# Kernel tuning notes

Hardware: AMD Instinct MI355X
Metric: run time of the kernel (lower is better)

The kernel has to match this reference:

```python
import jax, jax.numpy as jnp
import numpy as np

L = 65536   # sequence length (keys/values)
D = 512     # embed dim (hardcoded in source)
H = 4       # heads
HD = 128    # head dim

def _ln(x, g, b):
    m = jnp.mean(x, -1, keepdims=True)
    v = jnp.var(x, -1, keepdims=True)
    return (x - m) * jax.lax.rsqrt(v + 1e-5) * g + b

def setup_inputs() -> dict:
    key = jax.random.key(0)
    ks = jax.random.split(key, 6)
    s = 0.02
    return {
        "x": jax.random.normal(ks[0], (L, D), jnp.float32),
        "w_in": jax.random.normal(ks[1], (3 * D, D), jnp.float32) * s,
        "b_in": jnp.zeros((3 * D,), jnp.float32),
        "w_out": jax.random.normal(ks[2], (D, D), jnp.float32) * s,
        "b_out": jnp.zeros((D,), jnp.float32),
        "w1": jax.random.normal(ks[3], (D, D), jnp.float32) * s,
        "b1": jnp.zeros((D,), jnp.float32),
        "w2": jax.random.normal(ks[4], (D, D), jnp.float32) * s,
        "b2": jnp.zeros((D,), jnp.float32),
        "g1": jnp.ones((D,), jnp.float32),
        "be1": jnp.zeros((D,), jnp.float32),
        "g2": jnp.ones((D,), jnp.float32),
        "be2": jnp.zeros((D,), jnp.float32),
    }

def reference(x, w_in, b_in, w_out, b_out, w1, b1, w2, b2, g1, be1, g2, be2):
    xn = _ln(x, g1, be1)                               # [L, D]
    q = xn[:1] @ w_in[:D].T + b_in[:D]                 # [1, D] single-row query
    k = xn @ w_in[D:2 * D].T + b_in[D:2 * D]           # [L, D]
    v = xn @ w_in[2 * D:].T + b_in[2 * D:]             # [L, D]
    qh = q.reshape(H, HD)                              # [H, HD]
    kh = k.reshape(L, H, HD)
    vh = v.reshape(L, H, HD)
    scores = jnp.einsum('hd,lhd->hl', qh, kh) * (1.0 / np.sqrt(HD))  # [H, L]
    attn = jax.nn.softmax(scores, axis=-1)
    o = jnp.einsum('hl,lhd->hd', attn, vh).reshape(1, D)             # [1, D]
    o = o @ w_out.T + b_out
    y = x[:1] + o                                      # residual keeps only row 0
    yn = _ln(y, g2, be2)
    h = jax.nn.relu(yn @ w1.T + b1)
    return y + h @ w2.T + b2                           # [1, D]
```

## Files before the change

### kernel.cpp

```cpp
#include <hip/hip_runtime.h>
#include <math.h>

#define LL 65536
#define DD 512
#define NH 4
#define HDIM 128


__device__ __forceinline__ float dot4(float4 a, float4 b) {
    return a.x * b.x + a.y * b.y + a.z * b.z + a.w * b.w;
}
__device__ __forceinline__ float wred(float v) {
#pragma unroll
    for (int m = 32; m; m >>= 1) v += __shfl_xor(v, m, 64);
    return v;
}
__device__ __forceinline__ float4 f4fma(float4 acc, float s, float4 v) {
    acc.x += s * v.x; acc.y += s * v.y; acc.z += s * v.z; acc.w += s * v.w;
    return acc;
}
__device__ __forceinline__ float4 f4sfma(float4 acc, float c, float s, float4 v) {
    acc.x = acc.x * c + s * v.x; acc.y = acc.y * c + s * v.y;
    acc.z = acc.z * c + s * v.z; acc.w = acc.w * c + s * v.w;
    return acc;
}
__device__ __forceinline__ float4 f4scale(float4 a, float s) {
    a.x *= s; a.y *= s; a.z *= s; a.w *= s; return a;
}
__device__ __forceinline__ float4 lnrm4(float4 v, float m, float r, float4 g, float4 b) {
    float4 o;
    o.x = (v.x - m) * r * g.x + b.x; o.y = (v.y - m) * r * g.y + b.y;
    o.z = (v.z - m) * r * g.z + b.z; o.w = (v.w - m) * r * g.w + b.w;
    return o;
}

__global__ __launch_bounds__(256) void kA1(const float* __restrict__ x,
                                           const float* __restrict__ w_in,
                                           const float* __restrict__ b_in,
                                           const float* __restrict__ g1,
                                           const float* __restrict__ be1,
                                           float* __restrict__ ws) {
    int lane = threadIdx.x & 63;
    int j = blockIdx.x * 4 + (threadIdx.x >> 6);
    const float4* x4 = (const float4*)x;
    float4 a = x4[lane], b = x4[64 + lane];
    float ps = a.x + a.y + a.z + a.w + b.x + b.y + b.z + b.w;
    float pss = dot4(a, a) + dot4(b, b);
    ps = wred(ps); pss = wred(pss);
    float m = ps * (1.f / 512.f);
    float r = rsqrtf(pss * (1.f / 512.f) - m * m + 1e-5f);
    const float4* g4 = (const float4*)g1;
    const float4* bb4 = (const float4*)be1;
    float4 xna = lnrm4(a, m, r, g4[lane], bb4[lane]);
    float4 xnb = lnrm4(b, m, r, g4[64 + lane], bb4[64 + lane]);
    const float4* wr = (const float4*)(w_in + (size_t)j * DD);
    float acc = dot4(wr[lane], xna) + dot4(wr[64 + lane], xnb);
    acc = wred(acc);
    if (lane == 0) ws[j] = acc + b_in[j];
}

__global__ __launch_bounds__(512) void kA2(const float* __restrict__ w_in,
                                           const float* __restrict__ g1,
                                           float* __restrict__ ws) {
    __shared__ float qh[128];
    __shared__ float red[512];
    int h = blockIdx.x, tid = threadIdx.x;
    if (tid < 128) qh[tid] = ws[h * HDIM + tid];
    __syncthreads();
    const float* wk = w_in + (size_t)(DD + h * HDIM) * DD + tid;
    float acc = 0.f;
#pragma unroll 4
    for (int d = 0; d < HDIM; ++d) acc += qh[d] * wk[(size_t)d * DD];
    acc *= 0.088388347648318447f;
    float qg = acc * g1[tid];
    ws[512 + h * 512 + tid] = qg;
    red[tid] = qg;
    __syncthreads();
    for (int s = 256; s; s >>= 1) {
        if (tid < s) red[tid] += red[tid + s];
        __syncthreads();
    }
    if (tid == 0) ws[2560 + h] = red[0];
}

__global__ __launch_bounds__(512) void kB(const float* __restrict__ x,
                                          float* __restrict__ ws) {
    __shared__ float lds[16384];
    int tid = threadIdx.x, lane = tid & 63, w = tid >> 6;
    const float4* qkg4 = (const float4*)(ws + 512);
    float4 qa[4], qb[4];
    float qs[4];
#pragma unroll
    for (int h = 0; h < 4; ++h) {
        qa[h] = qkg4[h * 128 + lane];
        qb[h] = qkg4[h * 128 + 64 + lane];
        qs[h] = ws[2560 + h];
    }
    float mx[4], sm[4], w2a[4];
    float4 Wa[4], Wb[4];
#pragma unroll
    for (int h = 0; h < 4; ++h) {
        mx[h] = -INFINITY; sm[h] = 0.f; w2a[h] = 0.f;
        Wa[h] = make_float4(0.f, 0.f, 0.f, 0.f);
        Wb[h] = make_float4(0.f, 0.f, 0.f, 0.f);
    }
    size_t row0 = ((size_t)blockIdx.x * 8 + w) * 32;
    const float4* xb = (const float4*)x + row0 * 128;
    for (int r = 0; r < 32; ++r) {
        float4 xa = xb[r * 128 + lane];
        float4 xc = xb[r * 128 + 64 + lane];
        float ps = xa.x + xa.y + xa.z + xa.w + xc.x + xc.y + xc.z + xc.w;
        float pss = dot4(xa, xa) + dot4(xc, xc);
        float p0 = dot4(xa, qa[0]) + dot4(xc, qb[0]);
        float p1 = dot4(xa, qa[1]) + dot4(xc, qb[1]);
        float p2 = dot4(xa, qa[2]) + dot4(xc, qb[2]);
        float p3 = dot4(xa, qa[3]) + dot4(xc, qb[3]);
        ps = wred(ps); pss = wred(pss);
        p0 = wred(p0); p1 = wred(p1); p2 = wred(p2); p3 = wred(p3);
        float m = ps * (1.f / 512.f);
        float rr = rsqrtf(pss * (1.f / 512.f) - m * m + 1e-5f);
        float rm = rr * m;
        float pd[4] = {p0, p1, p2, p3};
#pragma unroll
        for (int h = 0; h < 4; ++h) {
            float s = rr * pd[h] - rm * qs[h];
            if (s <= mx[h]) {
                float p = __expf(s - mx[h]);
                sm[h] += p;
                w2a[h] += p * rm;
                float pr = p * rr;
                Wa[h] = f4fma(Wa[h], pr, xa);
                Wb[h] = f4fma(Wb[h], pr, xc);
            } else {
                float cc = __expf(mx[h] - s);
                sm[h] = sm[h] * cc + 1.f;
                w2a[h] = w2a[h] * cc + rm;
                Wa[h] = f4sfma(Wa[h], cc, rr, xa);
                Wb[h] = f4sfma(Wb[h], cc, rr, xc);
                mx[h] = s;
            }
        }
    }
    float* lmx = lds; float* lsm = lds + 32; float* lw2 = lds + 64;
    if (lane == 0) {
#pragma unroll
        for (int h = 0; h < 4; ++h) {
            lmx[w * 4 + h] = mx[h];
            lsm[w * 4 + h] = sm[h];
            lw2[w * 4 + h] = w2a[h];
        }
    }
    __syncthreads();
    float bmx[4], f[4];
#pragma unroll
    for (int h = 0; h < 4; ++h) {
        float bm = lmx[h];
#pragma unroll
        for (int ww = 1; ww < 8; ++ww) bm = fmaxf(bm, lmx[ww * 4 + h]);
        bmx[h] = bm;
        f[h] = __expf(mx[h] - bm);
    }
    if (tid == 0) {
#pragma unroll
        for (int h = 0; h < 4; ++h) {
            float bs = 0.f, bw = 0.f;
            for (int ww = 0; ww < 8; ++ww) {
                float ff = __expf(lmx[ww * 4 + h] - bmx[h]);
                bs += lsm[ww * 4 + h] * ff;
                bw += lw2[ww * 4 + h] * ff;
            }
            ws[8192 + blockIdx.x * 4 + h] = bmx[h];
            ws[9216 + blockIdx.x * 4 + h] = bs;
            ws[10240 + blockIdx.x * 4 + h] = bw;
        }
    }
    __syncthreads();
    float4* lw4 = (float4*)(lds + w * 2048);
#pragma unroll
    for (int h = 0; h < 4; ++h) {
        lw4[h * 128 + lane] = f4scale(Wa[h], f[h]);
        lw4[h * 128 + 64 + lane] = f4scale(Wb[h], f[h]);
    }
    __syncthreads();
    float* Wout = ws + 12288 + (size_t)blockIdx.x * 2048;
    for (int i = tid; i < 2048; i += 512) {
        float a = lds[i] + lds[2048 + i] + lds[4096 + i] + lds[6144 + i] +
                  lds[8192 + i] + lds[10240 + i] + lds[12288 + i] + lds[14336 + i];
        Wout[i] = a;
    }
}

__global__ __launch_bounds__(256) void kC0(float* __restrict__ ws) {
    __shared__ float red[256];
    int tid = threadIdx.x;
    for (int h = 0; h < 4; ++h) {
        float vm = ws[8192 + tid * 4 + h];
        float vs = ws[9216 + tid * 4 + h];
        float vw = ws[10240 + tid * 4 + h];
        red[tid] = vm; __syncthreads();
        for (int s = 128; s; s >>= 1) {
            if (tid < s) red[tid] = fmaxf(red[tid], red[tid + s]);
            __syncthreads();
        }
        float bm = red[0]; __syncthreads();
        float ff = __expf(vm - bm);
        red[tid] = vs * ff; __syncthreads();
        for (int s = 128; s; s >>= 1) {
            if (tid < s) red[tid] += red[tid + s];
            __syncthreads();
        }
        float smg = red[0]; __syncthreads();
        red[tid] = vw * ff; __syncthreads();
        for (int s = 128; s; s >>= 1) {
            if (tid < s) red[tid] += red[tid + s];
            __syncthreads();
        }
        float w2g = red[0]; __syncthreads();
        if (tid == 0) {
            ws[2564 + h] = bm;
            ws[2568 + h] = 1.f / smg;
            ws[2572 + h] = w2g / smg;
        }
    }
}

__global__ __launch_bounds__(256) void kC1(const float* __restrict__ g1,
                                           const float* __restrict__ be1,
                                           float* __restrict__ ws) {
    __shared__ float ef[256];
    int tid = threadIdx.x;
    int t = blockIdx.x * 256 + tid;
    int h = t >> 9, e = t & 511;
    ef[tid] = __expf(ws[8192 + tid * 4 + h] - ws[2564 + h]);
    __syncthreads();
    const float* Wb = ws + 12288 + h * 512 + e;
    float acc = 0.f;
#pragma unroll 8
    for (int b = 0; b < 256; ++b) acc += Wb[(size_t)b * 2048] * ef[b];
    float cv = g1[e] * (acc * ws[2568 + h] - ws[2572 + h]) + be1[e];
    ws[2576 + t] = cv;
}

__global__ __launch_bounds__(256) void kD1(const float* __restrict__ w_in,
                                           const float* __restrict__ b_in,
                                           float* __restrict__ ws) {
    int lane = threadIdx.x & 63;
    int j = blockIdx.x * 4 + (threadIdx.x >> 6);
    const float4* wr = (const float4*)(w_in + (size_t)(2 * DD + j) * DD);
    const float4* cr = (const float4*)(ws + 2576 + (j >> 7) * 512);
    float acc = dot4(wr[lane], cr[lane]) + dot4(wr[64 + lane], cr[64 + lane]);
    acc = wred(acc);
    if (lane == 0) ws[4624 + j] = acc + b_in[2 * DD + j];
}

__global__ __launch_bounds__(256) void kD2(const float* __restrict__ x,
                                           const float* __restrict__ w_out,
                                           const float* __restrict__ b_out,
                                           float* __restrict__ ws) {
    int lane = threadIdx.x & 63;
    int j = blockIdx.x * 4 + (threadIdx.x >> 6);
    const float4* wr = (const float4*)(w_out + (size_t)j * DD);
    const float4* o4 = (const float4*)(ws + 4624);
    float acc = dot4(wr[lane], o4[lane]) + dot4(wr[64 + lane], o4[64 + lane]);
    acc = wred(acc);
    if (lane == 0) ws[5136 + j] = x[j] + acc + b_out[j];
}

__global__ __launch_bounds__(512) void kD2b(float* __restrict__ ws) {
    __shared__ float red[512];
    int tid = threadIdx.x;
    float v = ws[5136 + tid];
    red[tid] = v; __syncthreads();
    for (int s = 256; s; s >>= 1) {
        if (tid < s) red[tid] += red[tid + s];
        __syncthreads();
    }
    float m = red[0] * (1.f / 512.f);
    __syncthreads();
    red[tid] = v * v; __syncthreads();
    for (int s = 256; s; s >>= 1) {
        if (tid < s) red[tid] += red[tid + s];
        __syncthreads();
    }
    float var = red[0] * (1.f / 512.f) - m * m;
    if (tid == 0) { ws[5648] = m; ws[5649] = rsqrtf(var + 1e-5f); }
}

__global__ __launch_bounds__(256) void kD3(const float* __restrict__ w1,
                                           const float* __restrict__ b1,
                                           const float* __restrict__ g2,
                                           const float* __restrict__ be2,
                                           float* __restrict__ ws) {
    int lane = threadIdx.x & 63;
    int j = blockIdx.x * 4 + (threadIdx.x >> 6);
    float m2 = ws[5648], r2 = ws[5649];
    const float4* y4 = (const float4*)(ws + 5136);
    const float4* g4 = (const float4*)g2;
    const float4* b4 = (const float4*)be2;
    float4 yna = lnrm4(y4[lane], m2, r2, g4[lane], b4[lane]);
    float4 ynb = lnrm4(y4[64 + lane], m2, r2, g4[64 + lane], b4[64 + lane]);
    const float4* wr = (const float4*)(w1 + (size_t)j * DD);
    float acc = dot4(wr[lane], yna) + dot4(wr[64 + lane], ynb);
    acc = wred(acc);
    if (lane == 0) ws[5664 + j] = fmaxf(acc + b1[j], 0.f);
}

__global__ __launch_bounds__(256) void kD4(const float* __restrict__ w2,
                                           const float* __restrict__ b2,
                                           const float* __restrict__ ws,
                                           float* __restrict__ out) {
    int lane = threadIdx.x & 63;
    int j = blockIdx.x * 4 + (threadIdx.x >> 6);
    const float4* h4 = (const float4*)(ws + 5664);
    const float4* wr = (const float4*)(w2 + (size_t)j * DD);
    float acc = dot4(wr[lane], h4[lane]) + dot4(wr[64 + lane], h4[64 + lane]);
    acc = wred(acc);
    if (lane == 0) out[j] = ws[5136 + j] + acc + b2[j];
}

extern "C" void kernel_launch(void* const* d_in, const int* in_sizes, int n_in,
                              void* d_out, int out_size, void* d_ws, size_t ws_size,
                              hipStream_t stream) {
    (void)in_sizes; (void)n_in; (void)out_size; (void)ws_size;
    const float* x = (const float*)d_in[0];
    const float* w_in = (const float*)d_in[1];
    const float* b_in = (const float*)d_in[2];
    const float* w_out = (const float*)d_in[3];
    const float* b_out = (const float*)d_in[4];
    const float* w1 = (const float*)d_in[5];
    const float* b1 = (const float*)d_in[6];
    const float* w2 = (const float*)d_in[7];
    const float* b2 = (const float*)d_in[8];
    const float* g1 = (const float*)d_in[9];
    const float* be1 = (const float*)d_in[10];
    const float* g2 = (const float*)d_in[11];
    const float* be2 = (const float*)d_in[12];
    float* ws = (float*)d_ws;
    float* out = (float*)d_out;

    hipLaunchKernelGGL(kA1, dim3(128), dim3(256), 0, stream, x, w_in, b_in, g1, be1, ws);
    hipLaunchKernelGGL(kA2, dim3(4), dim3(512), 0, stream, w_in, g1, ws);
    hipLaunchKernelGGL(kB, dim3(256), dim3(512), 0, stream, x, ws);
    hipLaunchKernelGGL(kC0, dim3(1), dim3(256), 0, stream, ws);
    hipLaunchKernelGGL(kC1, dim3(8), dim3(256), 0, stream, g1, be1, ws);
    hipLaunchKernelGGL(kD1, dim3(128), dim3(256), 0, stream, w_in, b_in, ws);
    hipLaunchKernelGGL(kD2, dim3(128), dim3(256), 0, stream, x, w_out, b_out, ws);
    hipLaunchKernelGGL(kD2b, dim3(1), dim3(512), 0, stream, ws);
    hipLaunchKernelGGL(kD3, dim3(128), dim3(256), 0, stream, w1, b1, g2, be2, ws);
    hipLaunchKernelGGL(kD4, dim3(128), dim3(256), 0, stream, w2, b2, ws, out);
}
```

Before: 281.3 us.

## Drop online-softmax max tracking and fuse reduction stages into fewer kernels

```diff
diff --git a/kernel.cpp b/kernel.cpp
--- a/kernel.cpp
+++ b/kernel.cpp
@@ -19,20 +19,25 @@
     acc.x += s * v.x; acc.y += s * v.y; acc.z += s * v.z; acc.w += s * v.w;
     return acc;
 }
-__device__ __forceinline__ float4 f4sfma(float4 acc, float c, float s, float4 v) {
-    acc.x = acc.x * c + s * v.x; acc.y = acc.y * c + s * v.y;
-    acc.z = acc.z * c + s * v.z; acc.w = acc.w * c + s * v.w;
-    return acc;
-}
-__device__ __forceinline__ float4 f4scale(float4 a, float s) {
-    a.x *= s; a.y *= s; a.z *= s; a.w *= s; return a;
-}
+__device__ __forceinline__ float4 f4add(float4 a, float4 b) {
+    a.x += b.x; a.y += b.y; a.z += b.z; a.w += b.w; return a;
+}
+__device__ __forceinline__ float4 f4muls(float4 a, float4 g, float s) {
+    a.x *= g.x * s; a.y *= g.y * s; a.z *= g.z * s; a.w *= g.w * s; return a;
+}
+__device__ __forceinline__ float hsum4(float4 a) { return a.x + a.y + a.z + a.w; }
 __device__ __forceinline__ float4 lnrm4(float4 v, float m, float r, float4 g, float4 b) {
     float4 o;
     o.x = (v.x - m) * r * g.x + b.x; o.y = (v.y - m) * r * g.y + b.y;
     o.z = (v.z - m) * r * g.z + b.z; o.w = (v.w - m) * r * g.w + b.w;
     return o;
 }
+__device__ __forceinline__ float4 caff4(float4 c, float inv, float w2t, float4 g, float4 b) {
+    float4 o;
+    o.x = g.x * (c.x * inv - w2t) + b.x; o.y = g.y * (c.y * inv - w2t) + b.y;
+    o.z = g.z * (c.z * inv - w2t) + b.z; o.w = g.w * (c.w * inv - w2t) + b.w;
+    return o;
+}
 
 __global__ __launch_bounds__(256) void kA1(const float* __restrict__ x,
                                            const float* __restrict__ w_in,
@@ -44,7 +49,7 @@
     int j = blockIdx.x * 4 + (threadIdx.x >> 6);
     const float4* x4 = (const float4*)x;
     float4 a = x4[lane], b = x4[64 + lane];
-    float ps = a.x + a.y + a.z + a.w + b.x + b.y + b.z + b.w;
+    float ps = hsum4(a) + hsum4(b);
     float pss = dot4(a, a) + dot4(b, b);
     ps = wred(ps); pss = wred(pss);
     float m = ps * (1.f / 512.f);
@@ -60,56 +65,56 @@
 }
 
 __global__ __launch_bounds__(512) void kA2(const float* __restrict__ w_in,
-                                           const float* __restrict__ g1,
-                                           float* __restrict__ ws) {
-    __shared__ float qh[128];
-    __shared__ float red[512];
-    int h = blockIdx.x, tid = threadIdx.x;
-    if (tid < 128) qh[tid] = ws[h * HDIM + tid];
-    __syncthreads();
-    const float* wk = w_in + (size_t)(DD + h * HDIM) * DD + tid;
+                                           float* __restrict__ ws) {
+    __shared__ float qh[32];
+    int bi = blockIdx.x, tid = threadIdx.x;
+    int h = bi >> 2, c = bi & 3;
+    if (tid < 32) qh[tid] = ws[h * HDIM + c * 32 + tid];
+    if (tid < 128) ws[9216 + bi * 128 + tid] = 0.f;
+    __syncthreads();
+    const float* wk = w_in + (size_t)(DD + h * HDIM + c * 32) * DD + tid;
     float acc = 0.f;
-#pragma unroll 4
-    for (int d = 0; d < HDIM; ++d) acc += qh[d] * wk[(size_t)d * DD];
-    acc *= 0.088388347648318447f;
-    float qg = acc * g1[tid];
-    ws[512 + h * 512 + tid] = qg;
-    red[tid] = qg;
-    __syncthreads();
-    for (int s = 256; s; s >>= 1) {
-        if (tid < s) red[tid] += red[tid + s];
-        __syncthreads();
-    }
-    if (tid == 0) ws[2560 + h] = red[0];
+#pragma unroll
+    for (int d = 0; d < 32; ++d) acc += qh[d] * wk[(size_t)d * DD];
+    ws[1024 + c * 2048 + h * 512 + tid] = acc;
 }
 
 __global__ __launch_bounds__(512) void kB(const float* __restrict__ x,
+                                          const float* __restrict__ g1,
                                           float* __restrict__ ws) {
     __shared__ float lds[16384];
     int tid = threadIdx.x, lane = tid & 63, w = tid >> 6;
-    const float4* qkg4 = (const float4*)(ws + 512);
+    const float4* p4 = (const float4*)(ws + 1024);
+    const float4* g4 = (const float4*)g1;
+    const float scale = 0.088388347648318447f;
+    float4 ga = g4[lane], gb = g4[64 + lane];
     float4 qa[4], qb[4];
     float qs[4];
 #pragma unroll
     for (int h = 0; h < 4; ++h) {
-        qa[h] = qkg4[h * 128 + lane];
-        qb[h] = qkg4[h * 128 + 64 + lane];
-        qs[h] = ws[2560 + h];
-    }
-    float mx[4], sm[4], w2a[4];
+        float4 sa = f4add(f4add(p4[h * 128 + lane], p4[512 + h * 128 + lane]),
+                          f4add(p4[1024 + h * 128 + lane], p4[1536 + h * 128 + lane]));
+        float4 sb = f4add(f4add(p4[h * 128 + 64 + lane], p4[512 + h * 128 + 64 + lane]),
+                          f4add(p4[1024 + h * 128 + 64 + lane], p4[1536 + h * 128 + 64 + lane]));
+        qa[h] = f4muls(sa, ga, scale);
+        qb[h] = f4muls(sb, gb, scale);
+        qs[h] = wred(hsum4(qa[h]) + hsum4(qb[h]));
+    }
+    float sm[4], w2a[4];
     float4 Wa[4], Wb[4];
 #pragma unroll
     for (int h = 0; h < 4; ++h) {
-        mx[h] = -INFINITY; sm[h] = 0.f; w2a[h] = 0.f;
+        sm[h] = 0.f; w2a[h] = 0.f;
         Wa[h] = make_float4(0.f, 0.f, 0.f, 0.f);
         Wb[h] = make_float4(0.f, 0.f, 0.f, 0.f);
     }
-    size_t row0 = ((size_t)blockIdx.x * 8 + w) * 32;
+    size_t row0 = ((size_t)blockIdx.x * 8 + w) * 16;
     const float4* xb = (const float4*)x + row0 * 128;
-    for (int r = 0; r < 32; ++r) {
-        float4 xa = xb[r * 128 + lane];
-        float4 xc = xb[r * 128 + 64 + lane];
-        float ps = xa.x + xa.y + xa.z + xa.w + xc.x + xc.y + xc.z + xc.w;
+    float4 nxa = xb[lane], nxc = xb[64 + lane];
+    for (int r = 0; r < 16; ++r) {
+        float4 xa = nxa, xc = nxc;
+        if (r < 15) { nxa = xb[(r + 1) * 128 + lane]; nxc = xb[(r + 1) * 128 + 64 + lane]; }
+        float ps = hsum4(xa) + hsum4(xc);
         float pss = dot4(xa, xa) + dot4(xc, xc);
         float p0 = dot4(xa, qa[0]) + dot4(xc, qb[0]);
         float p1 = dot4(xa, qa[1]) + dot4(xc, qb[1]);
@@ -124,65 +129,42 @@
 #pragma unroll
         for (int h = 0; h < 4; ++h) {
             float s = rr * pd[h] - rm * qs[h];
-            if (s <= mx[h]) {
-                float p = __expf(s - mx[h]);
-                sm[h] += p;
-                w2a[h] += p * rm;
-                float pr = p * rr;
-                Wa[h] = f4fma(Wa[h], pr, xa);
-                Wb[h] = f4fma(Wb[h], pr, xc);
-            } else {
-                float cc = __expf(mx[h] - s);
-                sm[h] = sm[h] * cc + 1.f;
-                w2a[h] = w2a[h] * cc + rm;
-                Wa[h] = f4sfma(Wa[h], cc, rr, xa);
-                Wb[h] = f4sfma(Wb[h], cc, rr, xc);
-                mx[h] = s;
-            }
+            float p = __expf(s);
+            sm[h] += p;
+            w2a[h] += p * rm;
+            float pr = p * rr;
+            Wa[h] = f4fma(Wa[h], pr, xa);
+            Wb[h] = f4fma(Wb[h], pr, xc);
         }
     }
-    float* lmx = lds; float* lsm = lds + 32; float* lw2 = lds + 64;
     if (lane == 0) {
 #pragma unroll
         for (int h = 0; h < 4; ++h) {
-            lmx[w * 4 + h] = mx[h];
-            lsm[w * 4 + h] = sm[h];
-            lw2[w * 4 + h] = w2a[h];
+            lds[w * 4 + h] = sm[h];
+            lds[32 + w * 4 + h] = w2a[h];
         }
     }
     __syncthreads();
-    float bmx[4], f[4];
+    if (tid < 8) {
+        int h = tid & 3;
+        float a = 0.f;
+        if (tid < 4) {
+            for (int ww = 0; ww < 8; ++ww) a += lds[ww * 4 + h];
+            ws[16384 + blockIdx.x * 4 + h] = a;
+        } else {
+            for (int ww = 0; ww < 8; ++ww) a += lds[32 + ww * 4 + h];
+            ws[18432 + blockIdx.x * 4 + h] = a;
+        }
+    }
+    __syncthreads();
+    float4* lw4 = (float4*)(lds + w * 2048);
 #pragma unroll
     for (int h = 0; h < 4; ++h) {
-        float bm = lmx[h];
-#pragma unroll
-        for (int ww = 1; ww < 8; ++ww) bm = fmaxf(bm, lmx[ww * 4 + h]);
-        bmx[h] = bm;
-        f[h] = __expf(mx[h] - bm);
-    }
-    if (tid == 0) {
-#pragma unroll
-        for (int h = 0; h < 4; ++h) {
-            float bs = 0.f, bw = 0.f;
-            for (int ww = 0; ww < 8; ++ww) {
-                float ff = __expf(lmx[ww * 4 + h] - bmx[h]);
-                bs += lsm[ww * 4 + h] * ff;
-                bw += lw2[ww * 4 + h] * ff;
-            }
-            ws[8192 + blockIdx.x * 4 + h] = bmx[h];
-            ws[9216 + blockIdx.x * 4 + h] = bs;
-            ws[10240 + blockIdx.x * 4 + h] = bw;
-        }
-    }
-    __syncthreads();
-    float4* lw4 = (float4*)(lds + w * 2048);
-#pragma unroll
-    for (int h = 0; h < 4; ++h) {
-        lw4[h * 128 + lane] = f4scale(Wa[h], f[h]);
-        lw4[h * 128 + 64 + lane] = f4scale(Wb[h], f[h]);
-    }
-    __syncthreads();
-    float* Wout = ws + 12288 + (size_t)blockIdx.x * 2048;
+        lw4[h * 128 + lane] = Wa[h];
+        lw4[h * 128 + 64 + lane] = Wb[h];
+    }
+    __syncthreads();
+    float* Wout = ws + 20480 + (size_t)blockIdx.x * 2048;
     for (int i = tid; i < 2048; i += 512) {
         float a = lds[i] + lds[2048 + i] + lds[4096 + i] + lds[6144 + i] +
                   lds[8192 + i] + lds[10240 + i] + lds[12288 + i] + lds[14336 + i];
@@ -190,67 +172,43 @@
     }
 }
 
-__global__ __launch_bounds__(256) void kC0(float* __restrict__ ws) {
-    __shared__ float red[256];
-    int tid = threadIdx.x;
-    for (int h = 0; h < 4; ++h) {
-        float vm = ws[8192 + tid * 4 + h];
-        float vs = ws[9216 + tid * 4 + h];
-        float vw = ws[10240 + tid * 4 + h];
-        red[tid] = vm; __syncthreads();
-        for (int s = 128; s; s >>= 1) {
-            if (tid < s) red[tid] = fmaxf(red[tid], red[tid + s]);
-            __syncthreads();
-        }
-        float bm = red[0]; __syncthreads();
-        float ff = __expf(vm - bm);
-        red[tid] = vs * ff; __syncthreads();
-        for (int s = 128; s; s >>= 1) {
-            if (tid < s) red[tid] += red[tid + s];
-            __syncthreads();
-        }
-        float smg = red[0]; __syncthreads();
-        red[tid] = vw * ff; __syncthreads();
-        for (int s = 128; s; s >>= 1) {
-            if (tid < s) red[tid] += red[tid + s];
-            __syncthreads();
-        }
-        float w2g = red[0]; __syncthreads();
-        if (tid == 0) {
-            ws[2564 + h] = bm;
-            ws[2568 + h] = 1.f / smg;
-            ws[2572 + h] = w2g / smg;
-        }
-    }
-}
-
-__global__ __launch_bounds__(256) void kC1(const float* __restrict__ g1,
-                                           const float* __restrict__ be1,
-                                           float* __restrict__ ws) {
-    __shared__ float ef[256];
-    int tid = threadIdx.x;
-    int t = blockIdx.x * 256 + tid;
-    int h = t >> 9, e = t & 511;
-    ef[tid] = __expf(ws[8192 + tid * 4 + h] - ws[2564 + h]);
-    __syncthreads();
-    const float* Wb = ws + 12288 + h * 512 + e;
+__global__ __launch_bounds__(256) void kC1(float* __restrict__ ws) {
+    int g = blockIdx.x * 256 + threadIdx.x;
+    int col = g & 2047, chunk = g >> 11;
+    const float* Wb = ws + 20480 + (size_t)chunk * 32 * 2048 + col;
     float acc = 0.f;
 #pragma unroll 8
-    for (int b = 0; b < 256; ++b) acc += Wb[(size_t)b * 2048] * ef[b];
-    float cv = g1[e] * (acc * ws[2568 + h] - ws[2572 + h]) + be1[e];
-    ws[2576 + t] = cv;
+    for (int b = 0; b < 32; ++b) acc += Wb[(size_t)b * 2048];
+    atomicAdd(&ws[9216 + col], acc);
 }
 
 __global__ __launch_bounds__(256) void kD1(const float* __restrict__ w_in,
                                            const float* __restrict__ b_in,
-                                           float* __restrict__ ws) {
-    int lane = threadIdx.x & 63;
-    int j = blockIdx.x * 4 + (threadIdx.x >> 6);
+                                           const float* __restrict__ g1,
+                                           const float* __restrict__ be1,
+                                           float* __restrict__ ws) {
+    __shared__ float sred[16];
+    int tid = threadIdx.x, lane = tid & 63, w = tid >> 6;
+    int j = blockIdx.x * 4 + w;
+    int h = j >> 7;
+    float s1 = ws[16384 + tid * 4 + h] + ws[16384 + (tid + 256) * 4 + h];
+    float s2 = ws[18432 + tid * 4 + h] + ws[18432 + (tid + 256) * 4 + h];
+    s1 = wred(s1); s2 = wred(s2);
+    if (lane == 0) { sred[w * 2] = s1; sred[w * 2 + 1] = s2; }
+    __syncthreads();
+    float smg = sred[0] + sred[2] + sred[4] + sred[6];
+    float w2g = sred[1] + sred[3] + sred[5] + sred[7];
+    float inv = 1.f / smg;
+    float w2t = w2g * inv;
+    const float4* cr = (const float4*)(ws + 9216 + h * 512);
+    const float4* g14 = (const float4*)g1;
+    const float4* be14 = (const float4*)be1;
+    float4 ca = caff4(cr[lane], inv, w2t, g14[lane], be14[lane]);
+    float4 cb = caff4(cr[64 + lane], inv, w2t, g14[64 + lane], be14[64 + lane]);
     const float4* wr = (const float4*)(w_in + (size_t)(2 * DD + j) * DD);
-    const float4* cr = (const float4*)(ws + 2576 + (j >> 7) * 512);
-    float acc = dot4(wr[lane], cr[lane]) + dot4(wr[64 + lane], cr[64 + lane]);
-    acc = wred(acc);
-    if (lane == 0) ws[4624 + j] = acc + b_in[2 * DD + j];
+    float acc = dot4(wr[lane], ca) + dot4(wr[64 + lane], cb);
+    acc = wred(acc);
+    if (lane == 0) ws[11264 + j] = acc + b_in[2 * DD + j];
 }
 
 __global__ __launch_bounds__(256) void kD2(const float* __restrict__ x,
@@ -260,30 +218,10 @@
     int lane = threadIdx.x & 63;
     int j = blockIdx.x * 4 + (threadIdx.x >> 6);
     const float4* wr = (const float4*)(w_out + (size_t)j * DD);
-    const float4* o4 = (const float4*)(ws + 4624);
+    const float4* o4 = (const float4*)(ws + 11264);
     float acc = dot4(wr[lane], o4[lane]) + dot4(wr[64 + lane], o4[64 + lane]);
     acc = wred(acc);
-    if (lane == 0) ws[5136 + j] = x[j] + acc + b_out[j];
-}
-
-__global__ __launch_bounds__(512) void kD2b(float* __restrict__ ws) {
-    __shared__ float red[512];
-    int tid = threadIdx.x;
-    float v = ws[5136 + tid];
-    red[tid] = v; __syncthreads();
-    for (int s = 256; s; s >>= 1) {
-        if (tid < s) red[tid] += red[tid + s];
-        __syncthreads();
-    }
-    float m = red[0] * (1.f / 512.f);
-    __syncthreads();
-    red[tid] = v * v; __syncthreads();
-    for (int s = 256; s; s >>= 1) {
-        if (tid < s) red[tid] += red[tid + s];
-        __syncthreads();
-    }
-    float var = red[0] * (1.f / 512.f) - m * m;
-    if (tid == 0) { ws[5648] = m; ws[5649] = rsqrtf(var + 1e-5f); }
+    if (lane == 0) ws[11776 + j] = x[j] + acc + b_out[j];
 }
 
 __global__ __launch_bounds__(256) void kD3(const float* __restrict__ w1,
@@ -293,16 +231,21 @@
                                            float* __restrict__ ws) {
     int lane = threadIdx.x & 63;
     int j = blockIdx.x * 4 + (threadIdx.x >> 6);
-    float m2 = ws[5648], r2 = ws[5649];
-    const float4* y4 = (const float4*)(ws + 5136);
+    const float4* y4 = (const float4*)(ws + 11776);
+    float4 ya = y4[lane], yb = y4[64 + lane];
+    float ps = hsum4(ya) + hsum4(yb);
+    float pss = dot4(ya, ya) + dot4(yb, yb);
+    ps = wred(ps); pss = wred(pss);
+    float m2 = ps * (1.f / 512.f);
+    float r2 = rsqrtf(pss * (1.f / 512.f) - m2 * m2 + 1e-5f);
     const float4* g4 = (const float4*)g2;
     const float4* b4 = (const float4*)be2;
-    float4 yna = lnrm4(y4[lane], m2, r2, g4[lane], b4[lane]);
-    float4 ynb = lnrm4(y4[64 + lane], m2, r2, g4[64 + lane], b4[64 + lane]);
+    float4 yna = lnrm4(ya, m2, r2, g4[lane], b4[lane]);
+    float4 ynb = lnrm4(yb, m2, r2, g4[64 + lane], b4[64 + lane]);
     const float4* wr = (const float4*)(w1 + (size_t)j * DD);
     float acc = dot4(wr[lane], yna) + dot4(wr[64 + lane], ynb);
     acc = wred(acc);
-    if (lane == 0) ws[5664 + j] = fmaxf(acc + b1[j], 0.f);
+    if (lane == 0) ws[12288 + j] = fmaxf(acc + b1[j], 0.f);
 }
 
 __global__ __launch_bounds__(256) void kD4(const float* __restrict__ w2,
@@ -311,11 +254,11 @@
                                            float* __restrict__ out) {
     int lane = threadIdx.x & 63;
     int j = blockIdx.x * 4 + (threadIdx.x >> 6);
-    const float4* h4 = (const float4*)(ws + 5664);
+    const float4* h4 = (const float4*)(ws + 12288);
     const float4* wr = (const float4*)(w2 + (size_t)j * DD);
     float acc = dot4(wr[lane], h4[lane]) + dot4(wr[64 + lane], h4[64 + lane]);
     acc = wred(acc);
-    if (lane == 0) out[j] = ws[5136 + j] + acc + b2[j];
+    if (lane == 0) out[j] = ws[11776 + j] + acc + b2[j];
 }
 
 extern "C" void kernel_launch(void* const* d_in, const int* in_sizes, int n_in,
@@ -339,13 +282,11 @@
     float* out = (float*)d_out;
 
     hipLaunchKernelGGL(kA1, dim3(128), dim3(256), 0, stream, x, w_in, b_in, g1, be1, ws);
-    hipLaunchKernelGGL(kA2, dim3(4), dim3(512), 0, stream, w_in, g1, ws);
-    hipLaunchKernelGGL(kB, dim3(256), dim3(512), 0, stream, x, ws);
-    hipLaunchKernelGGL(kC0, dim3(1), dim3(256), 0, stream, ws);
-    hipLaunchKernelGGL(kC1, dim3(8), dim3(256), 0, stream, g1, be1, ws);
-    hipLaunchKernelGGL(kD1, dim3(128), dim3(256), 0, stream, w_in, b_in, ws);
+    hipLaunchKernelGGL(kA2, dim3(16), dim3(512), 0, stream, w_in, ws);
+    hipLaunchKernelGGL(kB, dim3(512), dim3(512), 0, stream, x, g1, ws);
+    hipLaunchKernelGGL(kC1, dim3(128), dim3(256), 0, stream, ws);
+    hipLaunchKernelGGL(kD1, dim3(128), dim3(256), 0, stream, w_in, b_in, g1, be1, ws);
     hipLaunchKernelGGL(kD2, dim3(128), dim3(256), 0, stream, x, w_out, b_out, ws);
-    hipLaunchKernelGGL(kD2b, dim3(1), dim3(512), 0, stream, ws);
     hipLaunchKernelGGL(kD3, dim3(128), dim3(256), 0, stream, w1, b1, g2, be2, ws);
     hipLaunchKernelGGL(kD4, dim3(128), dim3(256), 0, stream, w2, b2, ws, out);
 }
```

After: 239.1 us. 1.18x faster.
